# Performance work log

Measured on AMD Instinct MI355X. Metric: run time of the kernel, lower is better.

## Reference

```python
import jax, jax.numpy as jnp
import numpy as np

B, L, H = 256, 256, 1024
NUM_HEADS = 16
DIM_PER_HEAD = H // NUM_HEADS  # 64
# faithful to source: scale = (dim_per_head // num_heads) ** -0.5 = (64//16)**-0.5 = 0.5
SCALE = (DIM_PER_HEAD // NUM_HEADS) ** (-0.5)
LN_EPS = 1e-5


def setup_inputs() -> dict:
    key = jax.random.key(0)
    ks = jax.random.split(key, 12)
    s = 1.0 / np.sqrt(H)
    return {
        "key": jax.random.normal(ks[0], (B, L, H), dtype=jnp.float32),
        "value": jax.random.normal(ks[1], (B, L, H), dtype=jnp.float32),
        "query": jax.random.normal(ks[2], (B, 1, H), dtype=jnp.float32),
        "attn_mask": jax.random.randint(ks[3], (B, 1, L), 0, 2).astype(bool),
        "Wq": jax.random.uniform(ks[4], (H, H), jnp.float32, -s, s),
        "bq": jnp.zeros((H,), jnp.float32),
        "Wk": jax.random.uniform(ks[5], (H, H), jnp.float32, -s, s),
        "bk": jnp.zeros((H,), jnp.float32),
        "Wv": jax.random.uniform(ks[6], (H, H), jnp.float32, -s, s),
        "bv": jnp.zeros((H,), jnp.float32),
        "Wf": jax.random.uniform(ks[7], (H, H), jnp.float32, -s, s),
        "bf": jnp.zeros((H,), jnp.float32),
        "gamma": jnp.ones((H,), jnp.float32),
        "beta": jnp.zeros((H,), jnp.float32),
    }


def _split_heads(x):
    # [B, L, H] -> [B, heads, L, d]
    b, l, _ = x.shape
    return x.reshape(b, l, NUM_HEADS, DIM_PER_HEAD).transpose(0, 2, 1, 3)


def reference(key, value, query, attn_mask, Wq, bq, Wk, bk, Wv, bv, Wf, bf, gamma, beta):
    residual = query  # [B, 1, H]
    k = _split_heads(key @ Wk.T + bk)      # [B, h, L, d]
    v = _split_heads(value @ Wv.T + bv)    # [B, h, L, d]
    q = _split_heads(query @ Wq.T + bq)    # [B, h, 1, d]

    scores = jnp.einsum('bhqd,bhkd->bhqk', q, k) * SCALE  # [B, h, 1, L]
    mask = attn_mask[:, None, :, :]                       # [B, 1, 1, L]
    scores = jnp.where(mask, -jnp.inf, scores)
    attention = jax.nn.softmax(scores, axis=-1)           # [B, h, 1, L]

    context = jnp.einsum('bhqk,bhkd->bhqd', attention, v)  # [B, h, 1, d]
    context = context.transpose(0, 2, 1, 3).reshape(query.shape[0], -1, H)  # [B, 1, H]

    out = context @ Wf.T + bf
    x = residual + out
    mu = jnp.mean(x, axis=-1, keepdims=True)
    var = jnp.mean(jnp.square(x - mu), axis=-1, keepdims=True)
    out = (x - mu) * jax.lax.rsqrt(var + LN_EPS) * gamma + beta

    # attention returned as [B*heads, 1, L] like torch bmm layout
    attn_flat = attention.reshape(query.shape[0] * NUM_HEADS, 1, -1)
    return out, attn_flat
```

## Files before the change

kernel.cpp:

```cpp
#include <hip/hip_runtime.h>
#include <math.h>

#define BB 256
#define LL 256
#define HH 1024
#define NH 16
#define DD 64
#define SCALE 0.5f
#define LN_EPS 1e-5f
#define NEG_BIG (-3.402823466e38f)

__global__ __launch_bounds__(256) void t_tr(const float* __restrict__ in,
                                            float* __restrict__ out, int inRS,
                                            int outRS, int inPlane,
                                            int outPlane) {
  __shared__ float lds[64][68];
  const float* ip = in + (size_t)blockIdx.z * inPlane;
  float* op = out + (size_t)blockIdx.z * outPlane;
  const int rt = blockIdx.y, ct = blockIdx.x;
  const int lr = threadIdx.x >> 4;
  const int lc = (threadIdx.x & 15) * 4;
#pragma unroll
  for (int p = 0; p < 4; p++) {
    float4 v = *(const float4*)(ip + (size_t)(rt * 64 + p * 16 + lr) * inRS +
                                ct * 64 + lc);
    *(float4*)(&lds[p * 16 + lr][lc]) = v;
  }
  __syncthreads();
#pragma unroll
  for (int p = 0; p < 4; p++) {
    float4 v = make_float4(lds[lc + 0][p * 16 + lr], lds[lc + 1][p * 16 + lr],
                           lds[lc + 2][p * 16 + lr], lds[lc + 3][p * 16 + lr]);
    *(float4*)(op + (size_t)(ct * 64 + p * 16 + lr) * outRS + rt * 64 + lc) = v;
  }
}

__global__ __launch_bounds__(256) void k1_qproj(const float* __restrict__ Wq,
                                                const float* __restrict__ qTT,
                                                const float* __restrict__ bq,
                                                float* __restrict__ qT) {
  __shared__ float smem[10240];
  const int jt = blockIdx.x;
  const int boff = blockIdx.y * 8;
  const int t = threadIdx.x;
  const int g = __builtin_amdgcn_readfirstlane(t >> 6);
  const int ln = t & 63;
  float* kw = smem + g * 2560;
  const float* Wb = Wq + (size_t)(jt * 64) * HH;
  const int srow = ln >> 2, sc = ln & 3;

  float acc[8];
#pragma unroll
  for (int c = 0; c < 8; c++) acc[c] = 0.f;
  float4 pf[4];
#pragma unroll
  for (int p = 0; p < 4; p++)
    pf[p] = *(const float4*)(Wb + (size_t)(p * 16 + srow) * HH + g * 16 + sc * 4);
  int buf = 0;
  for (int T = 0; T < 16; T++) {
    float* kb = kw + buf * 1280;
#pragma unroll
    for (int p = 0; p < 4; p++)
      *(float4*)(kb + ((p * 16 + srow) * 5 + sc) * 4) = pf[p];
    if (T < 15) {
      const int off = (T + 1) * 64 + g * 16 + sc * 4;
#pragma unroll
      for (int p = 0; p < 4; p++)
        pf[p] = *(const float4*)(Wb + (size_t)(p * 16 + srow) * HH + off);
    }
    const int i0 = T * 64 + g * 16;
#pragma unroll
    for (int u = 0; u < 4; u++) {
      float4 kv = *(const float4*)(kb + (ln * 5 + u) * 4);
      const float* q0 = qTT + (size_t)(i0 + u * 4 + 0) * BB + boff;
      const float* q1 = qTT + (size_t)(i0 + u * 4 + 1) * BB + boff;
      const float* q2 = qTT + (size_t)(i0 + u * 4 + 2) * BB + boff;
      const float* q3 = qTT + (size_t)(i0 + u * 4 + 3) * BB + boff;
#pragma unroll
      for (int c = 0; c < 8; c++) {
        acc[c] = fmaf(kv.x, q0[c], acc[c]);
        acc[c] = fmaf(kv.y, q1[c], acc[c]);
        acc[c] = fmaf(kv.z, q2[c], acc[c]);
        acc[c] = fmaf(kv.w, q3[c], acc[c]);
      }
    }
    buf ^= 1;
  }
  __syncthreads();
  float* part = smem;
  *(float4*)(part + g * 768 + ln * 12 + 0) =
      make_float4(acc[0], acc[1], acc[2], acc[3]);
  *(float4*)(part + g * 768 + ln * 12 + 4) =
      make_float4(acc[4], acc[5], acc[6], acc[7]);
  __syncthreads();
  const int j = t & 63, c0 = (t >> 6) * 2;
  float v0 = 0.f, v1 = 0.f;
#pragma unroll
  for (int g2 = 0; g2 < 4; g2++) {
    v0 += part[g2 * 768 + j * 12 + c0];
    v1 += part[g2 * 768 + j * 12 + c0 + 1];
  }
  const int jg = jt * 64 + j;
  const float bias = bq[jg];
  *(float2*)(qT + (size_t)jg * BB + boff + c0) =
      make_float2(v0 + bias, v1 + bias);
}

__global__ __launch_bounds__(256) void k2_qk(const float* __restrict__ qT,
                                             const float* __restrict__ Wk,
                                             float* __restrict__ qkT) {
  const int h = blockIdx.y;
  const int it = blockIdx.x;
  const int il = threadIdx.x & 63;
  const int bs = __builtin_amdgcn_readfirstlane(threadIdx.x >> 6);
  const int i = it * 64 + il;
  const int boff = blockIdx.z * 64 + bs * 16;
  float acc[16];
#pragma unroll
  for (int k = 0; k < 16; k++) acc[k] = 0.f;
#pragma unroll 2
  for (int d = 0; d < DD; d++) {
    float wv = Wk[(size_t)(h * DD + d) * HH + i];
    const float* qrow = qT + (h * DD + d) * BB + boff;
#pragma unroll
    for (int k = 0; k < 16; k++) acc[k] = fmaf(qrow[k], wv, acc[k]);
  }
#pragma unroll
  for (int k = 0; k < 16; k++)
    qkT[(size_t)((boff + k) * NH + h) * HH + i] = SCALE * acc[k];
}

__global__ __launch_bounds__(256, 4) void k3a_scores(
    const float* __restrict__ key, const int* __restrict__ mask,
    const float* __restrict__ qkT, float* __restrict__ scoresT) {
  __shared__ float smem[10240];
  const int b = blockIdx.y;
  const int lt = blockIdx.x;
  const int t = threadIdx.x;
  const int g = __builtin_amdgcn_readfirstlane(t >> 6);
  const int lam = t & 63;
  float* kw = smem + g * 2560;
  const float* keyb = key + ((size_t)b * LL + lt * 64) * HH;
  const float* qkb = qkT + (size_t)b * (NH * HH);

  const int srow = lam >> 2;
  const int sc = lam & 3;

  float acc[16];
#pragma unroll
  for (int h = 0; h < NH; h++) acc[h] = 0.f;

  float4 pf[4];
#pragma unroll
  for (int j = 0; j < 4; j++)
    pf[j] = *(const float4*)(keyb + (size_t)(j * 16 + srow) * HH + g * 16 + sc * 4);

  int buf = 0;
  for (int T = 0; T < 16; T++) {
    float* kb = kw + buf * 1280;
#pragma unroll
    for (int j = 0; j < 4; j++)
      *(float4*)(kb + ((j * 16 + srow) * 5 + sc) * 4) = pf[j];
    if (T < 15) {
      const int off = (T + 1) * 64 + g * 16 + sc * 4;
#pragma unroll
      for (int j = 0; j < 4; j++)
        pf[j] = *(const float4*)(keyb + (size_t)(j * 16 + srow) * HH + off);
    }
    const int i0 = T * 64 + g * 16;
#pragma unroll
    for (int u = 0; u < 4; u++) {
      float4 kv = *(const float4*)(kb + (lam * 5 + u) * 4);
      const int ib = i0 + u * 4;
#pragma unroll
      for (int h = 0; h < NH; h++) {
        const float* qh = qkb + h * HH + ib;
        acc[h] = fmaf(kv.x, qh[0], acc[h]);
        acc[h] = fmaf(kv.y, qh[1], acc[h]);
        acc[h] = fmaf(kv.z, qh[2], acc[h]);
        acc[h] = fmaf(kv.w, qh[3], acc[h]);
      }
    }
    buf ^= 1;
  }

  __syncthreads();
  float* part = smem;
#pragma unroll
  for (int u = 0; u < 4; u++)
    *(float4*)(part + (g * 64 + lam) * 20 + u * 4) =
        make_float4(acc[u * 4], acc[u * 4 + 1], acc[u * 4 + 2], acc[u * 4 + 3]);
  __syncthreads();
  const int row = t & 63, hq = t >> 6;
  float4 s0 = *(const float4*)(part + (0 * 64 + row) * 20 + hq * 4);
  float4 s1 = *(const float4*)(part + (1 * 64 + row) * 20 + hq * 4);
  float4 s2 = *(const float4*)(part + (2 * 64 + row) * 20 + hq * 4);
  float4 s3 = *(const float4*)(part + (3 * 64 + row) * 20 + hq * 4);
  const int l = lt * 64 + row;
  const int mk = mask[b * LL + l];
  float o0 = mk ? NEG_BIG : (s0.x + s1.x + s2.x + s3.x);
  float o1 = mk ? NEG_BIG : (s0.y + s1.y + s2.y + s3.y);
  float o2 = mk ? NEG_BIG : (s0.z + s1.z + s2.z + s3.z);
  float o3 = mk ? NEG_BIG : (s0.w + s1.w + s2.w + s3.w);
  scoresT[(size_t)(b * NH + hq * 4 + 0) * LL + l] = o0;
  scoresT[(size_t)(b * NH + hq * 4 + 1) * LL + l] = o1;
  scoresT[(size_t)(b * NH + hq * 4 + 2) * LL + l] = o2;
  scoresT[(size_t)(b * NH + hq * 4 + 3) * LL + l] = o3;
}

__global__ __launch_bounds__(256) void k3b_softmax(float* __restrict__ attn) {
  const int r = blockIdx.x * 4 + (threadIdx.x >> 6);
  const int lane = threadIdx.x & 63;
  float* rowp = attn + (size_t)r * LL;
  float4 s = *(const float4*)(rowp + lane * 4);
  float m = fmaxf(fmaxf(s.x, s.y), fmaxf(s.z, s.w));
#pragma unroll
  for (int off = 32; off >= 1; off >>= 1) m = fmaxf(m, __shfl_xor(m, off));
  float ex = __expf(s.x - m), ey = __expf(s.y - m), ez = __expf(s.z - m),
        ew = __expf(s.w - m);
  float e = ex + ey + ez + ew;
#pragma unroll
  for (int off = 32; off >= 1; off >>= 1) e += __shfl_xor(e, off);
  float inv = 1.0f / e;
  *(float4*)(rowp + lane * 4) = make_float4(ex * inv, ey * inv, ez * inv, ew * inv);
}

__global__ __launch_bounds__(256, 4) void k3c_vbar(
    const float* __restrict__ value, const float* __restrict__ attn,
    float* __restrict__ vbar) {
  const int b = blockIdx.y;
  const int d = blockIdx.x * 256 + threadIdx.x;
  const float* ab = attn + (size_t)b * NH * LL;
  const float* valb = value + (size_t)b * LL * HH + d;
  float acc[16];
#pragma unroll
  for (int h = 0; h < NH; h++) acc[h] = 0.f;
  for (int l0 = 0; l0 < LL; l0 += 16) {
    float vv[16];
#pragma unroll
    for (int k = 0; k < 16; k++) vv[k] = valb[(size_t)(l0 + k) * HH];
#pragma unroll
    for (int h = 0; h < NH; h++) {
      const float4* ar = (const float4*)(ab + h * LL + l0);
      float4 a0 = ar[0], a1 = ar[1], a2 = ar[2], a3 = ar[3];
      acc[h] = fmaf(a0.x, vv[0], acc[h]);
      acc[h] = fmaf(a0.y, vv[1], acc[h]);
      acc[h] = fmaf(a0.z, vv[2], acc[h]);
      acc[h] = fmaf(a0.w, vv[3], acc[h]);
      acc[h] = fmaf(a1.x, vv[4], acc[h]);
      acc[h] = fmaf(a1.y, vv[5], acc[h]);
      acc[h] = fmaf(a1.z, vv[6], acc[h]);
      acc[h] = fmaf(a1.w, vv[7], acc[h]);
      acc[h] = fmaf(a2.x, vv[8], acc[h]);
      acc[h] = fmaf(a2.y, vv[9], acc[h]);
      acc[h] = fmaf(a2.z, vv[10], acc[h]);
      acc[h] = fmaf(a2.w, vv[11], acc[h]);
      acc[h] = fmaf(a3.x, vv[12], acc[h]);
      acc[h] = fmaf(a3.y, vv[13], acc[h]);
      acc[h] = fmaf(a3.z, vv[14], acc[h]);
      acc[h] = fmaf(a3.w, vv[15], acc[h]);
    }
  }
#pragma unroll
  for (int h = 0; h < NH; h++)
    vbar[((size_t)b * NH + h) * HH + d] = acc[h];
}

__global__ __launch_bounds__(256) void k4_ctx(const float* __restrict__ Wv,
                                              const float* __restrict__ vbarT,
                                              const float* __restrict__ bv,
                                              float* __restrict__ ctxT) {
  __shared__ float smem[10240];
  const int jt = blockIdx.x;
  const int boff = blockIdx.y * 8;
  const int t = threadIdx.x;
  const int g = __builtin_amdgcn_readfirstlane(t >> 6);
  const int ln = t & 63;
  float* kw = smem + g * 2560;
  const float* Wb = Wv + (size_t)(jt * 64) * HH;
  const float* vt = vbarT + (size_t)jt * HH * BB;
  const int srow = ln >> 2, sc = ln & 3;

  float acc[8];
#pragma unroll
  for (int c = 0; c < 8; c++) acc[c] = 0.f;
  float4 pf[4];
#pragma unroll
  for (int p = 0; p < 4; p++)
    pf[p] = *(const float4*)(Wb + (size_t)(p * 16 + srow) * HH + g * 16 + sc * 4);
  int buf = 0;
  for (int T = 0; T < 16; T++) {
    float* kb = kw + buf * 1280;
#pragma unroll
    for (int p = 0; p < 4; p++)
      *(float4*)(kb + ((p * 16 + srow) * 5 + sc) * 4) = pf[p];
    if (T < 15) {
      const int off = (T + 1) * 64 + g * 16 + sc * 4;
#pragma unroll
      for (int p = 0; p < 4; p++)
        pf[p] = *(const float4*)(Wb + (size_t)(p * 16 + srow) * HH + off);
    }
    const int i0 = T * 64 + g * 16;
#pragma unroll
    for (int u = 0; u < 4; u++) {
      float4 kv = *(const float4*)(kb + (ln * 5 + u) * 4);
      const float* q0 = vt + (size_t)(i0 + u * 4 + 0) * BB + boff;
      const float* q1 = vt + (size_t)(i0 + u * 4 + 1) * BB + boff;
      const float* q2 = vt + (size_t)(i0 + u * 4 + 2) * BB + boff;
      const float* q3 = vt + (size_t)(i0 + u * 4 + 3) * BB + boff;
#pragma unroll
      for (int c = 0; c < 8; c++) {
        acc[c] = fmaf(kv.x, q0[c], acc[c]);
        acc[c] = fmaf(kv.y, q1[c], acc[c]);
        acc[c] = fmaf(kv.z, q2[c], acc[c]);
        acc[c] = fmaf(kv.w, q3[c], acc[c]);
      }
    }
    buf ^= 1;
  }
  __syncthreads();
  float* part = smem;
  *(float4*)(part + g * 768 + ln * 12 + 0) =
      make_float4(acc[0], acc[1], acc[2], acc[3]);
  *(float4*)(part + g * 768 + ln * 12 + 4) =
      make_float4(acc[4], acc[5], acc[6], acc[7]);
  __syncthreads();
  const int j = t & 63, c0 = (t >> 6) * 2;
  float v0 = 0.f, v1 = 0.f;
#pragma unroll
  for (int g2 = 0; g2 < 4; g2++) {
    v0 += part[g2 * 768 + j * 12 + c0];
    v1 += part[g2 * 768 + j * 12 + c0 + 1];
  }
  const int jg = jt * 64 + j;
  const float bias = bv[jg];
  *(float2*)(ctxT + (size_t)jg * BB + boff + c0) =
      make_float2(v0 + bias, v1 + bias);
}

__global__ __launch_bounds__(256) void k5_outproj(
    const float* __restrict__ Wf, const float* __restrict__ ctxT,
    const float* __restrict__ bf, const float* __restrict__ query,
    float* __restrict__ xws) {
  __shared__ float smem[10240];
  const int jt = blockIdx.x;
  const int boff = blockIdx.y * 8;
  const int t = threadIdx.x;
  const int g = __builtin_amdgcn_readfirstlane(t >> 6);
  const int ln = t & 63;
  float* kw = smem + g * 2560;
  const float* Wb = Wf + (size_t)(jt * 64) * HH;
  const int srow = ln >> 2, sc = ln & 3;

  float acc[8];
#pragma unroll
  for (int c = 0; c < 8; c++) acc[c] = 0.f;
  float4 pf[4];
#pragma unroll
  for (int p = 0; p < 4; p++)
    pf[p] = *(const float4*)(Wb + (size_t)(p * 16 + srow) * HH + g * 16 + sc * 4);
  int buf = 0;
  for (int T = 0; T < 16; T++) {
    float* kb = kw + buf * 1280;
#pragma unroll
    for (int p = 0; p < 4; p++)
      *(float4*)(kb + ((p * 16 + srow) * 5 + sc) * 4) = pf[p];
    if (T < 15) {
      const int off = (T + 1) * 64 + g * 16 + sc * 4;
#pragma unroll
      for (int p = 0; p < 4; p++)
        pf[p] = *(const float4*)(Wb + (size_t)(p * 16 + srow) * HH + off);
    }
    const int i0 = T * 64 + g * 16;
#pragma unroll
    for (int u = 0; u < 4; u++) {
      float4 kv = *(const float4*)(kb + (ln * 5 + u) * 4);
      const float* q0 = ctxT + (size_t)(i0 + u * 4 + 0) * BB + boff;
      const float* q1 = ctxT + (size_t)(i0 + u * 4 + 1) * BB + boff;
      const float* q2 = ctxT + (size_t)(i0 + u * 4 + 2) * BB + boff;
      const float* q3 = ctxT + (size_t)(i0 + u * 4 + 3) * BB + boff;
#pragma unroll
      for (int c = 0; c < 8; c++) {
        acc[c] = fmaf(kv.x, q0[c], acc[c]);
        acc[c] = fmaf(kv.y, q1[c], acc[c]);
        acc[c] = fmaf(kv.z, q2[c], acc[c]);
        acc[c] = fmaf(kv.w, q3[c], acc[c]);
      }
    }
    buf ^= 1;
  }
  __syncthreads();
  float* part = smem;
  *(float4*)(part + g * 768 + ln * 12 + 0) =
      make_float4(acc[0], acc[1], acc[2], acc[3]);
  *(float4*)(part + g * 768 + ln * 12 + 4) =
      make_float4(acc[4], acc[5], acc[6], acc[7]);
  __syncthreads();
  const int j = t & 63, c0 = (t >> 6) * 2;
  float v0 = 0.f, v1 = 0.f;
#pragma unroll
  for (int g2 = 0; g2 < 4; g2++) {
    v0 += part[g2 * 768 + j * 12 + c0];
    v1 += part[g2 * 768 + j * 12 + c0 + 1];
  }
  const int jg = jt * 64 + j;
  const float bias = bf[jg];
  const int b0 = boff + c0;
  xws[(size_t)b0 * HH + jg] = v0 + bias + query[(size_t)b0 * HH + jg];
  xws[(size_t)(b0 + 1) * HH + jg] = v1 + bias + query[(size_t)(b0 + 1) * HH + jg];
}

__global__ __launch_bounds__(256) void k6_ln(const float* __restrict__ xws,
                                             const float* __restrict__ gamma,
                                             const float* __restrict__ beta,
                                             float* __restrict__ out0) {
  __shared__ float rb[8];
  const int b = blockIdx.x, t = threadIdx.x;
  float4 v = *(const float4*)(xws + (size_t)b * HH + 4 * t);
  float s = v.x + v.y + v.z + v.w;
#pragma unroll
  for (int off = 32; off >= 1; off >>= 1) s += __shfl_xor(s, off);
  if ((t & 63) == 0) rb[t >> 6] = s;
  __syncthreads();
  float mu = (rb[0] + rb[1] + rb[2] + rb[3]) * (1.0f / HH);
  float dx = v.x - mu, dy = v.y - mu, dz = v.z - mu, dw = v.w - mu;
  float q = dx * dx + dy * dy + dz * dz + dw * dw;
#pragma unroll
  for (int off = 32; off >= 1; off >>= 1) q += __shfl_xor(q, off);
  if ((t & 63) == 0) rb[4 + (t >> 6)] = q;
  __syncthreads();
  float var = (rb[4] + rb[5] + rb[6] + rb[7]) * (1.0f / HH);
  float rs = rsqrtf(var + LN_EPS);
  float4 gm = *(const float4*)(gamma + 4 * t);
  float4 bt = *(const float4*)(beta + 4 * t);
  float4 o;
  o.x = dx * rs * gm.x + bt.x;
  o.y = dy * rs * gm.y + bt.y;
  o.z = dz * rs * gm.z + bt.z;
  o.w = dw * rs * gm.w + bt.w;
  *(float4*)(out0 + (size_t)b * HH + 4 * t) = o;
}

extern "C" void kernel_launch(void* const* d_in, const int* in_sizes, int n_in,
                              void* d_out, int out_size, void* d_ws,
                              size_t ws_size, hipStream_t stream) {
  (void)in_sizes; (void)n_in; (void)out_size; (void)ws_size;
  const float* key = (const float*)d_in[0];
  const float* value = (const float*)d_in[1];
  const float* query = (const float*)d_in[2];
  const int* mask = (const int*)d_in[3];
  const float* Wq = (const float*)d_in[4];
  const float* bq = (const float*)d_in[5];
  const float* Wk = (const float*)d_in[6];
  const float* Wv = (const float*)d_in[8];
  const float* bv = (const float*)d_in[9];
  const float* Wf = (const float*)d_in[10];
  const float* bf = (const float*)d_in[11];
  const float* gamma = (const float*)d_in[12];
  const float* beta = (const float*)d_in[13];

  float* out0 = (float*)d_out;
  float* attnOut = out0 + BB * HH;

  char* ws = (char*)d_ws;
  float* qT = (float*)(ws);
  float* qTT = (float*)(ws + (1 << 20));
  float* qkT = (float*)(ws + (2 << 20));
  float* vbar = (float*)(ws + (18 << 20));
  float* vbarT = (float*)(ws + (34 << 20));
  float* ctxT = (float*)(ws + (50 << 20));
  float* xws = (float*)(ws + (51 << 20));

  t_tr<<<dim3(16, 4, 1), 256, 0, stream>>>(query, qTT, HH, BB, 0, 0);
  k1_qproj<<<dim3(16, 32), 256, 0, stream>>>(Wq, qTT, bq, qT);
  k2_qk<<<dim3(16, 16, 4), 256, 0, stream>>>(qT, Wk, qkT);
  k3a_scores<<<dim3(4, 256), 256, 0, stream>>>(key, mask, qkT, attnOut);
  k3b_softmax<<<dim3(1024), 256, 0, stream>>>(attnOut);
  k3c_vbar<<<dim3(4, 256), 256, 0, stream>>>(value, attnOut, vbar);
  t_tr<<<dim3(16, 4, 16), 256, 0, stream>>>(vbar, vbarT, NH * HH, BB, HH,
                                            HH * BB);
  k4_ctx<<<dim3(16, 32), 256, 0, stream>>>(Wv, vbarT, bv, ctxT);
  k5_outproj<<<dim3(16, 32), 256, 0, stream>>>(Wf, ctxT, bf, query, xws);
  k6_ln<<<dim3(256), 256, 0, stream>>>(xws, gamma, beta, out0);
}
```

Measured before the change: 430.9 us.

## Relayout qk into interleaved per-head chunks and stream key rows directly in scores kernel

Adds a relayout kernel that reorders the per-batch qk product so that 16 heads by 4 elements are contiguous for each 4-element block of the hidden dimension. The scores kernel then drops its LDS staging of key tiles: each thread reads its own key row straight from global memory with register double-buffering, and all threads read qk values at uniform addresses. The aim is to remove LDS traffic and barriers in the key stream and make the qk reads scalar or broadcast friendly. The cost is an extra kernel launch with an additional 16MB read and write pass, plus workspace buffers reused across stages. Per-thread row reads of key are strided rather than coalesced across lanes.

```diff
diff --git a/kernel.cpp b/kernel.cpp
--- a/kernel.cpp
+++ b/kernel.cpp
@@ -130,65 +130,84 @@
     qkT[(size_t)((boff + k) * NH + h) * HH + i] = SCALE * acc[k];
 }
 
+__global__ __launch_bounds__(256) void k2b_relayout(
+    const float* __restrict__ qkT, float* __restrict__ qkR) {
+  __shared__ float lds[16][268];
+  const int b = blockIdx.y, seg = blockIdx.x;
+  const int t = threadIdx.x;
+  const int row = t >> 4, l16 = t & 15;
+  const float* src = qkT + (size_t)b * 16384 + row * HH + seg * 256 + l16 * 16;
+#pragma unroll
+  for (int p = 0; p < 4; p++)
+    *(float4*)(&lds[row][l16 * 16 + p * 4]) = *(const float4*)(src + p * 4);
+  __syncthreads();
+  const int c = t & 63;
+  const int i4g = t >> 6;
+  const int h = c >> 2, i3 = c & 3;
+  float* dst = qkR + (size_t)b * 16384 + seg * 4096;
+#pragma unroll
+  for (int jj = 0; jj < 16; jj++) {
+    const int i4l = i4g * 16 + jj;
+    dst[i4l * 64 + c] = lds[h][i4l * 4 + i3];
+  }
+}
+
 __global__ __launch_bounds__(256, 4) void k3a_scores(
     const float* __restrict__ key, const int* __restrict__ mask,
-    const float* __restrict__ qkT, float* __restrict__ scoresT) {
-  __shared__ float smem[10240];
+    const float* __restrict__ qkR, float* __restrict__ scoresT) {
+  __shared__ float part[5120];
   const int b = blockIdx.y;
   const int lt = blockIdx.x;
   const int t = threadIdx.x;
   const int g = __builtin_amdgcn_readfirstlane(t >> 6);
-  const int lam = t & 63;
-  float* kw = smem + g * 2560;
-  const float* keyb = key + ((size_t)b * LL + lt * 64) * HH;
-  const float* qkb = qkT + (size_t)b * (NH * HH);
-
-  const int srow = lam >> 2;
-  const int sc = lam & 3;
+  const int ln = t & 63;
+  const float* keyrow = key + ((size_t)(b * LL + lt * 64 + ln)) * HH + g * 256;
+  const float* qkb = qkR + (size_t)b * 16384 + g * 4096;
 
   float acc[16];
 #pragma unroll
   for (int h = 0; h < NH; h++) acc[h] = 0.f;
 
-  float4 pf[4];
-#pragma unroll
-  for (int j = 0; j < 4; j++)
-    pf[j] = *(const float4*)(keyb + (size_t)(j * 16 + srow) * HH + g * 16 + sc * 4);
-
-  int buf = 0;
-  for (int T = 0; T < 16; T++) {
-    float* kb = kw + buf * 1280;
-#pragma unroll
-    for (int j = 0; j < 4; j++)
-      *(float4*)(kb + ((j * 16 + srow) * 5 + sc) * 4) = pf[j];
-    if (T < 15) {
-      const int off = (T + 1) * 64 + g * 16 + sc * 4;
-#pragma unroll
-      for (int j = 0; j < 4; j++)
-        pf[j] = *(const float4*)(keyb + (size_t)(j * 16 + srow) * HH + off);
-    }
-    const int i0 = T * 64 + g * 16;
-#pragma unroll
-    for (int u = 0; u < 4; u++) {
-      float4 kv = *(const float4*)(kb + (lam * 5 + u) * 4);
-      const int ib = i0 + u * 4;
-#pragma unroll
-      for (int h = 0; h < NH; h++) {
-        const float* qh = qkb + h * HH + ib;
-        acc[h] = fmaf(kv.x, qh[0], acc[h]);
-        acc[h] = fmaf(kv.y, qh[1], acc[h]);
-        acc[h] = fmaf(kv.z, qh[2], acc[h]);
-        acc[h] = fmaf(kv.w, qh[3], acc[h]);
-      }
-    }
-    buf ^= 1;
-  }
-
-  __syncthreads();
-  float* part = smem;
+  float4 p0 = *(const float4*)(keyrow + 0);
+  float4 p1 = *(const float4*)(keyrow + 4);
+  float4 p2 = *(const float4*)(keyrow + 8);
+  float4 p3 = *(const float4*)(keyrow + 12);
+
+  for (int c = 0; c < 16; c++) {
+    float4 k0 = p0, k1 = p1, k2 = p2, k3 = p3;
+    if (c < 15) {
+      const float* nx = keyrow + (c + 1) * 16;
+      p0 = *(const float4*)(nx + 0);
+      p1 = *(const float4*)(nx + 4);
+      p2 = *(const float4*)(nx + 8);
+      p3 = *(const float4*)(nx + 12);
+    }
+    const float* q = qkb + c * 256;
+#pragma unroll
+    for (int h = 0; h < NH; h++) {
+      const float* qh = q + h * 4;
+      acc[h] = fmaf(k0.x, qh[0], acc[h]);
+      acc[h] = fmaf(k0.y, qh[1], acc[h]);
+      acc[h] = fmaf(k0.z, qh[2], acc[h]);
+      acc[h] = fmaf(k0.w, qh[3], acc[h]);
+      acc[h] = fmaf(k1.x, qh[64], acc[h]);
+      acc[h] = fmaf(k1.y, qh[65], acc[h]);
+      acc[h] = fmaf(k1.z, qh[66], acc[h]);
+      acc[h] = fmaf(k1.w, qh[67], acc[h]);
+      acc[h] = fmaf(k2.x, qh[128], acc[h]);
+      acc[h] = fmaf(k2.y, qh[129], acc[h]);
+      acc[h] = fmaf(k2.z, qh[130], acc[h]);
+      acc[h] = fmaf(k2.w, qh[131], acc[h]);
+      acc[h] = fmaf(k3.x, qh[192], acc[h]);
+      acc[h] = fmaf(k3.y, qh[193], acc[h]);
+      acc[h] = fmaf(k3.z, qh[194], acc[h]);
+      acc[h] = fmaf(k3.w, qh[195], acc[h]);
+    }
+  }
+
 #pragma unroll
   for (int u = 0; u < 4; u++)
-    *(float4*)(part + (g * 64 + lam) * 20 + u * 4) =
+    *(float4*)(part + (g * 64 + ln) * 20 + u * 4) =
         make_float4(acc[u * 4], acc[u * 4 + 1], acc[u * 4 + 2], acc[u * 4 + 3]);
   __syncthreads();
   const int row = t & 63, hq = t >> 6;
@@ -466,15 +485,17 @@
   float* qT = (float*)(ws);
   float* qTT = (float*)(ws + (1 << 20));
   float* qkT = (float*)(ws + (2 << 20));
-  float* vbar = (float*)(ws + (18 << 20));
+  float* qkR = (float*)(ws + (18 << 20));
+  float* vbar = (float*)(ws + (2 << 20));
   float* vbarT = (float*)(ws + (34 << 20));
-  float* ctxT = (float*)(ws + (50 << 20));
-  float* xws = (float*)(ws + (51 << 20));
+  float* ctxT = (float*)(ws);
+  float* xws = (float*)(ws + (1 << 20));
 
   t_tr<<<dim3(16, 4, 1), 256, 0, stream>>>(query, qTT, HH, BB, 0, 0);
   k1_qproj<<<dim3(16, 32), 256, 0, stream>>>(Wq, qTT, bq, qT);
   k2_qk<<<dim3(16, 16, 4), 256, 0, stream>>>(qT, Wk, qkT);
-  k3a_scores<<<dim3(4, 256), 256, 0, stream>>>(key, mask, qkT, attnOut);
+  k2b_relayout<<<dim3(4, 256), 256, 0, stream>>>(qkT, qkR);
+  k3a_scores<<<dim3(4, 256), 256, 0, stream>>>(key, mask, qkR, attnOut);
   k3b_softmax<<<dim3(1024), 256, 0, stream>>>(attnOut);
   k3c_vbar<<<dim3(4, 256), 256, 0, stream>>>(value, attnOut, vbar);
   t_tr<<<dim3(16, 4, 16), 256, 0, stream>>>(vbar, vbarT, NH * HH, BB, HH,
```

Measured after the change: 358.8 us. -16.7%, faster.
